# Optimization experiments

Measured on AMD Instinct MI355X. Metric: run time of the kernel, lower is better.

Reference implementation:

```python
import jax, jax.numpy as jnp
import numpy as np

D_MODEL = 1024
N_HEADS = 16
HEAD_DIM = D_MODEL // N_HEADS
WINDOW = 256


def setup_inputs() -> dict:
    key = jax.random.key(0)
    kx, kq, ko = jax.random.split(key, 3)
    B, T = 4, 2048
    x = jax.random.normal(kx, (B, T, D_MODEL), dtype=jnp.float32)
    s = 1.0 / np.sqrt(D_MODEL)
    w_qkv = jax.random.normal(kq, (D_MODEL, 3 * D_MODEL), dtype=jnp.float32) * s
    w_out = jax.random.normal(ko, (D_MODEL, D_MODEL), dtype=jnp.float32) * s
    return {"x": x, "w_qkv": w_qkv, "w_out": w_out}


def reference(x, w_qkv, w_out):
    B, T, C = x.shape
    qkv = (x @ w_qkv).reshape(B, T, 3, N_HEADS, HEAD_DIM)
    q, k, v = qkv[:, :, 0], qkv[:, :, 1], qkv[:, :, 2]  # [B,T,H,D]
    # sliding-window causal mask: position i attends to j in (i-W, i]
    i = jnp.arange(T)[:, None]
    j = jnp.arange(T)[None, :]
    allowed = (j <= i) & (j > i - WINDOW)
    mask = jnp.where(allowed, 0.0, -jnp.inf).astype(x.dtype)  # [T,T]
    scale = 1.0 / np.sqrt(HEAD_DIM)
    scores = jnp.einsum('bqhd,bkhd->bhqk', q, k) * scale + mask
    attn = jax.nn.softmax(scores, axis=-1)
    out = jnp.einsum('bhqk,bkhd->bqhd', attn, v).reshape(B, T, C)
    return out @ w_out
```

## Files before the change

### kernel.cpp

```cpp
#include <hip/hip_runtime.h>

typedef unsigned short u16;
typedef __attribute__((ext_vector_type(8))) short bh8;
typedef __attribute__((ext_vector_type(4))) float f4;
typedef __attribute__((ext_vector_type(4))) unsigned short us4;

#define T_SEQ 2048
#define NHEADS 16
#define DHEAD 64
#define WIN 256

__device__ __forceinline__ float bf2f(u16 u) {
  union { unsigned int i; float f; } v; v.i = ((unsigned int)u) << 16; return v.f;
}
__device__ __forceinline__ u16 f2bf(float f) {
  unsigned int u = __float_as_uint(f);
  u = u + 0x7fffu + ((u >> 16) & 1u);
  return (u16)(u >> 16);
}
__device__ __forceinline__ void async16(const void* g, void* l) {
  void* gv = const_cast<void*>(g);
  __builtin_amdgcn_global_load_lds(
      (__attribute__((address_space(1))) void*)gv,
      (__attribute__((address_space(3))) void*)l, 16, 0, 0);
}

__global__ void detect_dtype(const void* x, int* flag) {
  if (threadIdx.x == 0 && blockIdx.x == 0) {
    const float* xf = (const float*)x;
    int ok = 1;
    for (int i = 0; i < 128; ++i) {
      float v = xf[i];
      float a = fabsf(v);
      if (!(a < 64.f)) { ok = 0; break; }
      if (!(v == 0.f || a > 1e-30f)) { ok = 0; break; }
    }
    *flag = ok;
  }
}

__global__ void xconv(const void* __restrict__ in, u16* __restrict__ out,
                      const int* __restrict__ flag, int n8) {
  const int i = blockIdx.x * 256 + threadIdx.x;
  if (i >= n8) return;
  const size_t e = (size_t)i * 8;
  if (*flag) {
    const float* f = (const float*)in;
    us4 o0, o1;
    #pragma unroll
    for (int u = 0; u < 4; ++u) { o0[u] = f2bf(f[e + u]); o1[u] = f2bf(f[e + 4 + u]); }
    *(us4*)&out[e] = o0; *(us4*)&out[e + 4] = o1;
  } else {
    *(us4*)&out[e]     = *(const us4*)&((const u16*)in)[e];
    *(us4*)&out[e + 4] = *(const us4*)&((const u16*)in)[e + 4];
  }
}

__global__ void transpose_conv(const void* __restrict__ in, u16* __restrict__ out,
                               int R, int C, const int* __restrict__ flag) {
  __shared__ alignas(16) u16 tile[32][33];
  const int isf = *flag;
  const int tx = threadIdx.x, ty = threadIdx.y;
  const int x  = blockIdx.x * 32 + tx;
  const int y0 = blockIdx.y * 32;
  #pragma unroll
  for (int i = ty; i < 32; i += 8) {
    u16 v;
    if (isf) v = f2bf(((const float*)in)[(size_t)(y0 + i) * C + x]);
    else     v = ((const u16*)in)[(size_t)(y0 + i) * C + x];
    tile[i][tx] = v;
  }
  __syncthreads();
  const int ox  = y0 + tx;
  const int oy0 = blockIdx.x * 32;
  #pragma unroll
  for (int i = ty; i < 32; i += 8)
    out[(size_t)(oy0 + i) * R + ox] = tile[tx][i];
}

template<bool ADYN, bool CDYN>
__global__ __launch_bounds__(256) void gemm_bt(
    const void* __restrict__ A, const u16* __restrict__ Bt,
    void* __restrict__ C, int N, int K, int lda, int ldc,
    const int* __restrict__ flag)
{
  __shared__ alignas(16) u16 As[128 * 32];
  __shared__ alignas(16) u16 Bs[128 * 32];

  const int isf  = ADYN ? *flag : 0;
  const int tid  = threadIdx.x;
  const int lane = tid & 63;
  const int w    = tid >> 6;
  const int wm   = (w >> 1) * 64;
  const int wn   = (w & 1) * 64;
  const int quad = lane >> 4;
  const int l16  = lane & 15;
  const int row0 = blockIdx.y * 128;
  const int col0 = blockIdx.x * 128;

  f4 acc[4][4] = {};

  const int srow = tid >> 2;
  const int scol = ((tid & 3) ^ ((tid >> 3) & 3)) * 8;
  const size_t aoff0 = (size_t)(row0 + srow) * lda + scol;
  const size_t aoff1 = (size_t)(row0 + 64 + srow) * lda + scol;
  const u16* gB0 = Bt + (size_t)(col0 + srow) * K + scol;
  const u16* gB1 = Bt + (size_t)(col0 + 64 + srow) * K + scol;
  u16* lA0 = As + tid * 8;
  u16* lA1 = As + 2048 + tid * 8;
  u16* lB0 = Bs + tid * 8;
  u16* lB1 = Bs + 2048 + tid * 8;

  const bool af32 = ADYN && isf;
  const int csw = (quad ^ ((l16 >> 1) & 3)) * 8;

  for (int k0 = 0; k0 < K; k0 += 32) {
    if (af32) {
      const float* Af = (const float*)A;
      f4 u00 = *(const f4*)(Af + aoff0 + k0);
      f4 u01 = *(const f4*)(Af + aoff0 + k0 + 4);
      f4 u10 = *(const f4*)(Af + aoff1 + k0);
      f4 u11 = *(const f4*)(Af + aoff1 + k0 + 4);
      bh8 a0, a1;
      #pragma unroll
      for (int u = 0; u < 4; ++u) {
        a0[u]     = (short)f2bf(u00[u]);
        a0[u + 4] = (short)f2bf(u01[u]);
        a1[u]     = (short)f2bf(u10[u]);
        a1[u + 4] = (short)f2bf(u11[u]);
      }
      __syncthreads();
      *(bh8*)lA0 = a0; *(bh8*)lA1 = a1;
      async16(gB0 + k0, lB0);
      async16(gB1 + k0, lB1);
    } else {
      const u16* A16 = (const u16*)A;
      __syncthreads();
      async16(A16 + aoff0 + k0, lA0);
      async16(A16 + aoff1 + k0, lA1);
      async16(gB0 + k0, lB0);
      async16(gB1 + k0, lB1);
    }
    __builtin_amdgcn_s_waitcnt(0);
    __syncthreads();

    bh8 af[4], bf[4];
    #pragma unroll
    for (int i = 0; i < 4; ++i)
      af[i] = *(const bh8*)(As + (wm + i * 16 + l16) * 32 + csw);
    #pragma unroll
    for (int j = 0; j < 4; ++j)
      bf[j] = *(const bh8*)(Bs + (wn + j * 16 + l16) * 32 + csw);
    #pragma unroll
    for (int i = 0; i < 4; ++i)
      #pragma unroll
      for (int j = 0; j < 4; ++j)
        acc[i][j] = __builtin_amdgcn_mfma_f32_16x16x32_bf16(af[i], bf[j], acc[i][j], 0, 0, 0);
  }

  const bool cf32 = CDYN && (*flag);
  #pragma unroll
  for (int i = 0; i < 4; ++i) {
    #pragma unroll
    for (int j = 0; j < 4; ++j) {
      const int rb = row0 + wm + i * 16 + quad * 4;
      const int cc = col0 + wn + j * 16 + l16;
      #pragma unroll
      for (int r = 0; r < 4; ++r) {
        if (cf32) ((float*)C)[(size_t)(rb + r) * ldc + cc] = acc[i][j][r];
        else      ((u16*)C)[(size_t)(rb + r) * ldc + cc]   = f2bf(acc[i][j][r]);
      }
    }
  }
}

__global__ __launch_bounds__(256) void attn_mfma(u16* __restrict__ qkv)
{
  __shared__ alignas(16) u16 Qs[64 * 72];
  __shared__ alignas(16) u16 Kt[64 * 72];
  __shared__ alignas(16) u16 Vt[64 * 72];
  __shared__ alignas(16) u16 Ps[64 * 72];

  const int tid  = threadIdx.x;
  const int lane = tid & 63;
  const int w    = tid >> 6;
  const int quad = lane >> 4;
  const int l16  = lane & 15;
  const int qb = blockIdx.x, h = blockIdx.y, b = blockIdx.z;
  const int qs = qb * 64;

  const u16* base = qkv + (size_t)b * T_SEQ * 3072 + h * 64;

  const int c8  = (tid & 7) * 8;
  const int r0s = tid >> 3;
  #pragma unroll
  for (int r = r0s; r < 64; r += 32)
    *(bh8*)&Qs[r * 72 + c8] = *(const bh8*)&base[(size_t)(qs + r) * 3072 + c8];

  f4 Oc[4] = {};
  float mst[4] = {-1e30f, -1e30f, -1e30f, -1e30f};
  float lst[4] = {0.f, 0.f, 0.f, 0.f};

  const int tmin = (qb >= 4) ? 0 : (4 - qb);

  for (int t = tmin; t < 5; ++t) {
    const int kt0 = qs - 256 + t * 64;
    __syncthreads();

    #pragma unroll
    for (int r = r0s; r < 64; r += 32) {
      *(bh8*)&Kt[r * 72 + c8] =
          *(const bh8*)&base[(size_t)(kt0 + r) * 3072 + 1024 + c8];
      bh8 v = *(const bh8*)&base[(size_t)(kt0 + r) * 3072 + 2048 + c8];
      const int kc = r >> 3, ki = r & 7;
      #pragma unroll
      for (int u = 0; u < 8; ++u) {
        const int d = c8 + u;
        Vt[d * 72 + ((kc ^ (d >> 3)) << 3) + ki] = (u16)v[u];
      }
    }
    __syncthreads();

    const int qrow = (w * 16 + l16) * 72;
    bh8 qa0 = *(const bh8*)&Qs[qrow + quad * 8];
    bh8 qa1 = *(const bh8*)&Qs[qrow + 32 + quad * 8];
    f4 S[4];
    #pragma unroll
    for (int kb = 0; kb < 4; ++kb) {
      const int krow = (kb * 16 + l16) * 72;
      bh8 kf0 = *(const bh8*)&Kt[krow + quad * 8];
      bh8 kf1 = *(const bh8*)&Kt[krow + 32 + quad * 8];
      f4 s = {};
      s = __builtin_amdgcn_mfma_f32_16x16x32_bf16(qa0, kf0, s, 0, 0, 0);
      s = __builtin_amdgcn_mfma_f32_16x16x32_bf16(qa1, kf1, s, 0, 0, 0);
      S[kb] = s;
    }

    const int iq0 = qs + w * 16 + quad * 4;
    float tmax[4] = {-1e30f, -1e30f, -1e30f, -1e30f};
    #pragma unroll
    for (int kb = 0; kb < 4; ++kb) {
      const int j = kt0 + kb * 16 + l16;
      #pragma unroll
      for (int rr = 0; rr < 4; ++rr) {
        const int i = iq0 + rr;
        float s = S[kb][rr] * 0.125f;
        const bool ok = (j <= i) && (j > i - WIN);
        s = ok ? s : -1e30f;
        S[kb][rr] = s;
        tmax[rr] = fmaxf(tmax[rr], s);
      }
    }
    #pragma unroll
    for (int off = 1; off < 16; off <<= 1)
      #pragma unroll
      for (int rr = 0; rr < 4; ++rr)
        tmax[rr] = fmaxf(tmax[rr], __shfl_xor(tmax[rr], off));

    float alpha[4], rsum[4];
    #pragma unroll
    for (int rr = 0; rr < 4; ++rr) {
      const float mnew = fmaxf(mst[rr], tmax[rr]);
      alpha[rr] = __expf(mst[rr] - mnew);
      mst[rr] = mnew;
      rsum[rr] = 0.f;
    }

    const int swq = quad >> 1;
    #pragma unroll
    for (int kb = 0; kb < 4; ++kb) {
      const int kc = kb * 2 + (l16 >> 3);
      const int ki = l16 & 7;
      #pragma unroll
      for (int rr = 0; rr < 4; ++rr) {
        const float sv = S[kb][rr];
        const float p = (sv > -0.5e30f) ? __expf(sv - mst[rr]) : 0.f;
        rsum[rr] += p;
        const int q = w * 16 + quad * 4 + rr;
        Ps[q * 72 + ((kc ^ swq) << 3) + ki] = f2bf(p);
      }
    }
    #pragma unroll
    for (int off = 1; off < 16; off <<= 1)
      #pragma unroll
      for (int rr = 0; rr < 4; ++rr)
        rsum[rr] += __shfl_xor(rsum[rr], off);
    #pragma unroll
    for (int rr = 0; rr < 4; ++rr)
      lst[rr] = lst[rr] * alpha[rr] + rsum[rr];

    #pragma unroll
    for (int db = 0; db < 4; ++db)
      #pragma unroll
      for (int rr = 0; rr < 4; ++rr)
        Oc[db][rr] *= alpha[rr];

    {
      const int q = w * 16 + l16;
      const int sw = (q >> 3) & 1;
      bh8 pa0 = *(const bh8*)&Ps[q * 72 + (((0 + quad) ^ sw) << 3)];
      bh8 pa1 = *(const bh8*)&Ps[q * 72 + (((4 + quad) ^ sw) << 3)];
      #pragma unroll
      for (int db = 0; db < 4; ++db) {
        const int d = db * 16 + l16;
        const int dsw = d >> 3;
        bh8 vb0 = *(const bh8*)&Vt[d * 72 + (((0 + quad) ^ dsw) << 3)];
        bh8 vb1 = *(const bh8*)&Vt[d * 72 + (((4 + quad) ^ dsw) << 3)];
        Oc[db] = __builtin_amdgcn_mfma_f32_16x16x32_bf16(pa0, vb0, Oc[db], 0, 0, 0);
        Oc[db] = __builtin_amdgcn_mfma_f32_16x16x32_bf16(pa1, vb1, Oc[db], 0, 0, 0);
      }
    }
  }

  u16* obase = (u16*)base;
  #pragma unroll
  for (int rr = 0; rr < 4; ++rr) {
    const int i = qs + w * 16 + quad * 4 + rr;
    const float inv = 1.f / lst[rr];
    #pragma unroll
    for (int db = 0; db < 4; ++db)
      obase[(size_t)i * 3072 + db * 16 + l16] = f2bf(Oc[db][rr] * inv);
  }
}

extern "C" void kernel_launch(void* const* d_in, const int* in_sizes, int n_in,
                              void* d_out, int out_size, void* d_ws, size_t ws_size,
                              hipStream_t stream) {
  const void* x     = d_in[0];
  const void* w_qkv = d_in[1];
  const void* w_out = d_in[2];

  const size_t SZ_QKV  = (size_t)8192 * 3072 * 2;
  const size_t SZ_XBF  = (size_t)8192 * 1024 * 2;
  const size_t SZ_WQ   = (size_t)3072 * 1024 * 2;
  const size_t SZ_WO   = (size_t)1024 * 1024 * 2;

  char* p = (char*)d_ws;
  u16* qkv   = (u16*)p; p += SZ_QKV;
  u16* wqkvT = (u16*)p; p += SZ_WQ;
  u16* woutT = (u16*)p; p += SZ_WO;
  int* flag  = (int*)p; p += 16;
  u16* xbf   = (u16*)p;
  const bool have_x = ws_size >= (SZ_QKV + SZ_WQ + SZ_WO + 16 + SZ_XBF);

  detect_dtype<<<1, 64, 0, stream>>>(x, flag);

  dim3 tb(32, 8);
  transpose_conv<<<dim3(96, 32), tb, 0, stream>>>(w_qkv, wqkvT, 1024, 3072, flag);
  transpose_conv<<<dim3(32, 32), tb, 0, stream>>>(w_out, woutT, 1024, 1024, flag);

  if (have_x) {
    xconv<<<dim3(4096), 256, 0, stream>>>(x, xbf, flag, 1048576);
    gemm_bt<false, false><<<dim3(24, 64), 256, 0, stream>>>(
        xbf, wqkvT, qkv, 3072, 1024, 1024, 3072, flag);
  } else {
    gemm_bt<true, false><<<dim3(24, 64), 256, 0, stream>>>(
        x, wqkvT, qkv, 3072, 1024, 1024, 3072, flag);
  }

  attn_mfma<<<dim3(32, NHEADS, 4), 256, 0, stream>>>(qkv);

  gemm_bt<false, true><<<dim3(8, 64), 256, 0, stream>>>(
      qkv, woutT, d_out, 1024, 1024, 3072, 1024, flag);
}
```

Before: 268.3 us.

## Merge weight transposes and x conversion into one prep kernel; deepen GEMM K-tile

Replaces the two transpose_conv launches and the xconv launch with one prep kernel that picks its job from the block index, removing two kernel launches. The GEMM K tile grows from 32 to 64 with a new 8-way XOR swizzle on the LDS layout, halving the number of barrier-synchronised load iterations. Launch bounds now request 4 blocks per CU. The larger tile doubles shared memory per block (32 KB), which may limit occupancy.

```diff
diff --git a/kernel.cpp b/kernel.cpp
--- a/kernel.cpp
+++ b/kernel.cpp
@@ -39,53 +39,62 @@
   }
 }
 
-__global__ void xconv(const void* __restrict__ in, u16* __restrict__ out,
-                      const int* __restrict__ flag, int n8) {
-  const int i = blockIdx.x * 256 + threadIdx.x;
-  if (i >= n8) return;
-  const size_t e = (size_t)i * 8;
-  if (*flag) {
-    const float* f = (const float*)in;
-    us4 o0, o1;
-    #pragma unroll
-    for (int u = 0; u < 4; ++u) { o0[u] = f2bf(f[e + u]); o1[u] = f2bf(f[e + 4 + u]); }
-    *(us4*)&out[e] = o0; *(us4*)&out[e + 4] = o1;
+__global__ __launch_bounds__(256) void prep(
+    const void* __restrict__ x, const void* __restrict__ w_qkv,
+    const void* __restrict__ w_out, u16* __restrict__ xbf,
+    u16* __restrict__ wqkvT, u16* __restrict__ woutT,
+    const int* __restrict__ flag, int have_x)
+{
+  const int bid = blockIdx.x;
+  const int tid = threadIdx.x;
+  const int isf = *flag;
+
+  if (bid < 4096) {
+    if (!have_x) return;
+    const size_t e = ((size_t)bid * 256 + tid) * 8;
+    if (isf) {
+      const float* f = (const float*)x;
+      us4 o0, o1;
+      #pragma unroll
+      for (int u = 0; u < 4; ++u) { o0[u] = f2bf(f[e + u]); o1[u] = f2bf(f[e + 4 + u]); }
+      *(us4*)&xbf[e] = o0; *(us4*)&xbf[e + 4] = o1;
+    } else {
+      *(us4*)&xbf[e]     = *(const us4*)&((const u16*)x)[e];
+      *(us4*)&xbf[e + 4] = *(const us4*)&((const u16*)x)[e + 4];
+    }
   } else {
-    *(us4*)&out[e]     = *(const us4*)&((const u16*)in)[e];
-    *(us4*)&out[e + 4] = *(const us4*)&((const u16*)in)[e + 4];
-  }
-}
-
-__global__ void transpose_conv(const void* __restrict__ in, u16* __restrict__ out,
-                               int R, int C, const int* __restrict__ flag) {
-  __shared__ alignas(16) u16 tile[32][33];
-  const int isf = *flag;
-  const int tx = threadIdx.x, ty = threadIdx.y;
-  const int x  = blockIdx.x * 32 + tx;
-  const int y0 = blockIdx.y * 32;
-  #pragma unroll
-  for (int i = ty; i < 32; i += 8) {
-    u16 v;
-    if (isf) v = f2bf(((const float*)in)[(size_t)(y0 + i) * C + x]);
-    else     v = ((const u16*)in)[(size_t)(y0 + i) * C + x];
-    tile[i][tx] = v;
-  }
-  __syncthreads();
-  const int ox  = y0 + tx;
-  const int oy0 = blockIdx.x * 32;
-  #pragma unroll
-  for (int i = ty; i < 32; i += 8)
-    out[(size_t)(oy0 + i) * R + ox] = tile[tx][i];
+    __shared__ alignas(16) u16 tile[32][33];
+    const void* in; u16* out; int C, bx, by;
+    if (bid < 4096 + 3072) { const int t = bid - 4096; in = w_qkv; out = wqkvT; C = 3072; bx = t % 96; by = t / 96; }
+    else                   { const int t = bid - 7168; in = w_out; out = woutT; C = 1024; bx = t % 32; by = t / 32; }
+    const int R = 1024;
+    const int tx = tid & 31, ty = tid >> 5;
+    const int xg = bx * 32 + tx;
+    const int y0 = by * 32;
+    #pragma unroll
+    for (int i = ty; i < 32; i += 8) {
+      u16 v;
+      if (isf) v = f2bf(((const float*)in)[(size_t)(y0 + i) * C + xg]);
+      else     v = ((const u16*)in)[(size_t)(y0 + i) * C + xg];
+      tile[i][tx] = v;
+    }
+    __syncthreads();
+    const int ox  = y0 + tx;
+    const int oy0 = bx * 32;
+    #pragma unroll
+    for (int i = ty; i < 32; i += 8)
+      out[(size_t)(oy0 + i) * R + ox] = tile[tx][i];
+  }
 }
 
 template<bool ADYN, bool CDYN>
-__global__ __launch_bounds__(256) void gemm_bt(
+__global__ __launch_bounds__(256, 4) void gemm_bt(
     const void* __restrict__ A, const u16* __restrict__ Bt,
     void* __restrict__ C, int N, int K, int lda, int ldc,
     const int* __restrict__ flag)
 {
-  __shared__ alignas(16) u16 As[128 * 32];
-  __shared__ alignas(16) u16 Bs[128 * 32];
+  __shared__ alignas(16) u16 As[128 * 64];
+  __shared__ alignas(16) u16 Bs[128 * 64];
 
   const int isf  = ADYN ? *flag : 0;
   const int tid  = threadIdx.x;
@@ -100,62 +109,68 @@
 
   f4 acc[4][4] = {};
 
-  const int srow = tid >> 2;
-  const int scol = ((tid & 3) ^ ((tid >> 3) & 3)) * 8;
-  const size_t aoff0 = (size_t)(row0 + srow) * lda + scol;
-  const size_t aoff1 = (size_t)(row0 + 64 + srow) * lda + scol;
-  const u16* gB0 = Bt + (size_t)(col0 + srow) * K + scol;
-  const u16* gB1 = Bt + (size_t)(col0 + 64 + srow) * K + scol;
-  u16* lA0 = As + tid * 8;
-  u16* lA1 = As + 2048 + tid * 8;
-  u16* lB0 = Bs + tid * 8;
-  u16* lB1 = Bs + 2048 + tid * 8;
+  size_t aoff[4]; const u16* bsrc[4]; int lofs[4];
+  #pragma unroll
+  for (int s = 0; s < 4; ++s) {
+    const int r  = s * 32 + (tid >> 3);
+    const int gc = (tid & 7) ^ (r & 7);
+    aoff[s] = (size_t)(row0 + r) * lda + gc * 8;
+    bsrc[s] = Bt + (size_t)(col0 + r) * K + gc * 8;
+    lofs[s] = s * 4096 + tid * 16;
+  }
 
   const bool af32 = ADYN && isf;
-  const int csw = (quad ^ ((l16 >> 1) & 3)) * 8;
-
-  for (int k0 = 0; k0 < K; k0 += 32) {
+
+  for (int k0 = 0; k0 < K; k0 += 64) {
     if (af32) {
       const float* Af = (const float*)A;
-      f4 u00 = *(const f4*)(Af + aoff0 + k0);
-      f4 u01 = *(const f4*)(Af + aoff0 + k0 + 4);
-      f4 u10 = *(const f4*)(Af + aoff1 + k0);
-      f4 u11 = *(const f4*)(Af + aoff1 + k0 + 4);
-      bh8 a0, a1;
-      #pragma unroll
-      for (int u = 0; u < 4; ++u) {
-        a0[u]     = (short)f2bf(u00[u]);
-        a0[u + 4] = (short)f2bf(u01[u]);
-        a1[u]     = (short)f2bf(u10[u]);
-        a1[u + 4] = (short)f2bf(u11[u]);
+      bh8 a[4];
+      #pragma unroll
+      for (int s = 0; s < 4; ++s) {
+        f4 u0 = *(const f4*)(Af + aoff[s] + k0);
+        f4 u1 = *(const f4*)(Af + aoff[s] + k0 + 4);
+        #pragma unroll
+        for (int u = 0; u < 4; ++u) { a[s][u] = (short)f2bf(u0[u]); a[s][u + 4] = (short)f2bf(u1[u]); }
       }
       __syncthreads();
-      *(bh8*)lA0 = a0; *(bh8*)lA1 = a1;
-      async16(gB0 + k0, lB0);
-      async16(gB1 + k0, lB1);
+      #pragma unroll
+      for (int s = 0; s < 4; ++s) {
+        *(bh8*)((char*)As + lofs[s]) = a[s];
+        async16(bsrc[s] + k0, (char*)Bs + lofs[s]);
+      }
     } else {
       const u16* A16 = (const u16*)A;
       __syncthreads();
-      async16(A16 + aoff0 + k0, lA0);
-      async16(A16 + aoff1 + k0, lA1);
-      async16(gB0 + k0, lB0);
-      async16(gB1 + k0, lB1);
+      #pragma unroll
+      for (int s = 0; s < 4; ++s) {
+        async16(A16 + aoff[s] + k0, (char*)As + lofs[s]);
+        async16(bsrc[s] + k0,       (char*)Bs + lofs[s]);
+      }
     }
     __builtin_amdgcn_s_waitcnt(0);
     __syncthreads();
 
-    bh8 af[4], bf[4];
-    #pragma unroll
-    for (int i = 0; i < 4; ++i)
-      af[i] = *(const bh8*)(As + (wm + i * 16 + l16) * 32 + csw);
-    #pragma unroll
-    for (int j = 0; j < 4; ++j)
-      bf[j] = *(const bh8*)(Bs + (wn + j * 16 + l16) * 32 + csw);
-    #pragma unroll
-    for (int i = 0; i < 4; ++i)
-      #pragma unroll
-      for (int j = 0; j < 4; ++j)
-        acc[i][j] = __builtin_amdgcn_mfma_f32_16x16x32_bf16(af[i], bf[j], acc[i][j], 0, 0, 0);
+    #pragma unroll
+    for (int ks = 0; ks < 2; ++ks) {
+      bh8 af[4], bf[4];
+      #pragma unroll
+      for (int i = 0; i < 4; ++i) {
+        const int row = wm + i * 16 + l16;
+        const int lc  = (ks * 4 + quad) ^ (row & 7);
+        af[i] = *(const bh8*)(As + row * 64 + lc * 8);
+      }
+      #pragma unroll
+      for (int j = 0; j < 4; ++j) {
+        const int row = wn + j * 16 + l16;
+        const int lc  = (ks * 4 + quad) ^ (row & 7);
+        bf[j] = *(const bh8*)(Bs + row * 64 + lc * 8);
+      }
+      #pragma unroll
+      for (int i = 0; i < 4; ++i)
+        #pragma unroll
+        for (int j = 0; j < 4; ++j)
+          acc[i][j] = __builtin_amdgcn_mfma_f32_16x16x32_bf16(af[i], bf[j], acc[i][j], 0, 0, 0);
+    }
   }
 
   const bool cf32 = CDYN && (*flag);
@@ -345,12 +360,10 @@
 
   detect_dtype<<<1, 64, 0, stream>>>(x, flag);
 
-  dim3 tb(32, 8);
-  transpose_conv<<<dim3(96, 32), tb, 0, stream>>>(w_qkv, wqkvT, 1024, 3072, flag);
-  transpose_conv<<<dim3(32, 32), tb, 0, stream>>>(w_out, woutT, 1024, 1024, flag);
+  prep<<<dim3(8192), 256, 0, stream>>>(x, w_qkv, w_out, xbf, wqkvT, woutT,
+                                       flag, have_x ? 1 : 0);
 
   if (have_x) {
-    xconv<<<dim3(4096), 256, 0, stream>>>(x, xbf, flag, 1048576);
     gemm_bt<false, false><<<dim3(24, 64), 256, 0, stream>>>(
         xbf, wqkvT, qkv, 3072, 1024, 1024, 3072, flag);
   } else {
```

Measured after the change: 239.3 us. 1.12x faster.
